# Optimization experiments

Hardware: AMD Instinct MI355X
Metric: run time of the kernel (lower is better)

The kernel has to match this reference:

```python
import jax, jax.numpy as jnp
import numpy as np

BLOCK_SIZE = 1024
OUTLIER_SIGMA = 3.0
OUT_FEATURES = 11008
IN_FEATURES = 4096
TOKENS = 64


def _quantize_mixed_np(W):
    """Faithful numpy port of quantize_mixed (BLOCK_SIZE divides numel exactly here)."""
    flat = W.astype(np.float32).reshape(-1)
    nb = flat.size // BLOCK_SIZE
    blocks = flat.reshape(nb, BLOCK_SIZE)
    mu = blocks.mean(axis=1, keepdims=True)
    sig = np.maximum(blocks.std(axis=1, ddof=1, keepdims=True), 1e-8)  # torch.std is unbiased
    outlier = np.abs(blocks - mu) > OUTLIER_SIGMA * sig
    abs_max = np.maximum(np.abs(np.where(outlier, 0.0, blocks)).max(axis=1), 1e-8)
    scales = (abs_max / 127.0).astype(np.float16)
    q = np.clip(np.round(blocks / abs_max[:, None] * 127.0), -127, 127).astype(np.int8)
    all_pos = np.arange(nb, dtype=np.int64)[:, None] * BLOCK_SIZE + np.arange(BLOCK_SIZE, dtype=np.int64)[None, :]
    int8_data = q[~outlier]                      # row-major == torch order
    fp16_data = blocks[outlier].astype(np.float16)
    int8_pos = all_pos[~outlier].astype(np.int32)
    fp16_pos = all_pos[outlier].astype(np.int32)
    block_idx = np.nonzero(~outlier)[0].astype(np.int32)  # block index per int8 value
    return int8_data, fp16_data, scales, int8_pos, fp16_pos, block_idx


def setup_inputs() -> dict:
    key = jax.random.key(0)
    k_x, k_b = jax.random.split(key)
    rng = np.random.default_rng(0)
    W = (rng.standard_normal((OUT_FEATURES, IN_FEATURES)) * 0.02).astype(np.float32)
    int8_data, fp16_data, scales, int8_pos, fp16_pos, block_idx = _quantize_mixed_np(W)
    x = jax.random.normal(k_x, (TOKENS, IN_FEATURES), dtype=jnp.float16)
    bias = jax.random.normal(k_b, (OUT_FEATURES,), dtype=jnp.float16) * jnp.float16(0.02)
    return {
        "x": x,
        "int8_data": jnp.asarray(int8_data),
        "fp16_data": jnp.asarray(fp16_data),
        "scales": jnp.asarray(scales),
        "bias": bias,
        "int8_pos": jnp.asarray(int8_pos),
        "fp16_pos": jnp.asarray(fp16_pos),
        "block_idx": jnp.asarray(block_idx),
    }


def reference(x, int8_data, fp16_data, scales, bias, int8_pos, fp16_pos, block_idx):
    out_features = bias.shape[0]
    in_features = x.shape[1]
    numel = out_features * in_features  # divisible by BLOCK_SIZE for these dims
    # dequantize_mixed: scatter fp16 outliers and dequantized int8 values into flat fp16 buffer
    flat = jnp.zeros((numel,), dtype=jnp.float16)
    flat = flat.at[fp16_pos].set(fp16_data)
    flat = flat.at[int8_pos].set(int8_data.astype(jnp.float16) * scales[block_idx])
    W = flat.reshape(out_features, in_features)
    # F.linear(x, W, bias) in fp16
    return jnp.dot(x.astype(jnp.float16), W.T) + bias
```

## Files before the change

kernel.cpp:

```cpp
#include <hip/hip_runtime.h>
#include <hip/hip_fp16.h>

#define TOK   64
#define INF   4096
#define OUTF  11008
#define NUMEL (OUTF * INF)
#define NSLC  (NUMEL / 64)
#define NBLK  (OUTF / 16)
#define KSPL  4
#define NCH   4
#define OUTN  (TOK * OUTF)

typedef __attribute__((ext_vector_type(8))) _Float16 half8;
typedef __attribute__((ext_vector_type(4))) _Float16 half4;
typedef __attribute__((ext_vector_type(4))) float floatx4;
typedef __attribute__((ext_vector_type(4), aligned(4))) int int4u;
typedef __attribute__((ext_vector_type(4))) int int4a;

#define BPAD 264

__global__ __launch_bounds__(256) void precompute_kernel(
    const float* __restrict__ x, const int* __restrict__ fppos, int nf,
    _Float16* __restrict__ x16, int* __restrict__ meta) {
  const int t = blockIdx.x * 256 + threadIdx.x;
  if (t < (TOK * INF) / 4) {
    const floatx4 f = *(const floatx4*)&x[t * 4];
    half4 h;
    h[0] = (_Float16)f[0]; h[1] = (_Float16)f[1];
    h[2] = (_Float16)f[2]; h[3] = (_Float16)f[3];
    *(half4*)&x16[t * 4] = h;
  }
  if (t < NSLC) {
    const int target = t << 6;
    int lo = 0, hi = nf;
    while (lo < hi) {
      const int mid = (lo + hi) >> 1;
      if (fppos[mid] < target) lo = mid + 1; else hi = mid;
    }
    unsigned long long mask = 0ull;
    int j = lo;
    while (j < nf) {
      const int d = fppos[j] - target;
      if (d >= 64) break;
      mask |= 1ull << d;
      ++j;
    }
    int4a mv;
    mv[0] = lo;
    mv[1] = (int)(unsigned)(mask & 0xffffffffu);
    mv[2] = (int)(unsigned)(mask >> 32);
    mv[3] = 0;
    *(int4a*)&meta[t * 4] = mv;
  }
}

__device__ __forceinline__ void meta_window(const int p0, const int4a mv,
                                            int& i0, unsigned& m8) {
  const unsigned mlo = (unsigned)mv[1];
  const unsigned mhi = (unsigned)mv[2];
  const int off = p0 & 63;
  m8 = 0xffu & (off < 32 ? (mlo >> off) : (mhi >> (off - 32)));
  const unsigned bl = (off >= 32) ? mlo : (mlo & ((1u << off) - 1u));
  const unsigned bh = (off >= 32) ? (mhi & ((1u << (off - 32)) - 1u)) : 0u;
  i0 = p0 - mv[0] - (__popc(bl) + __popc(bh));
}

__device__ __forceinline__ half8 finish_slot(
    const unsigned m8, const int i0, const int p0, const float s,
    const int (&l)[8], const int* __restrict__ i8,
    const float* __restrict__ fpdat, const int n8) {
  const int f = (int)m8;
  float ov[8];
#pragma unroll
  for (int e = 0; e < 8; ++e) ov[e] = 0.f;
  if (f) {
    int fi = p0 - i0;
#pragma unroll
    for (int e = 0; e < 8; ++e) {
      if ((f >> e) & 1) { ov[e] = fpdat[fi]; ++fi; }
    }
  }

  half8 oh;
  if (i0 + 8 <= n8) {
    if (f == 0) {
#pragma unroll
      for (int e = 0; e < 8; ++e) oh[e] = (_Float16)((float)l[e] * s);
    } else {
      int q = 0;
#pragma unroll
      for (int e = 0; e < 8; ++e) {
        const int flg = (f >> e) & 1;
        int lv = l[0];
#pragma unroll
        for (int qq = 1; qq < 8; ++qq) lv = (q == qq) ? l[qq] : lv;
        oh[e] = flg ? (_Float16)ov[e] : (_Float16)((float)lv * s);
        q += 1 - flg;
      }
    }
  } else {
    int c = 0;
    const int m = n8 - 1;
#pragma unroll
    for (int e = 0; e < 8; ++e) {
      const int flg = (f >> e) & 1;
      int idx = i0 + e - c;
      idx = idx < 0 ? 0 : (idx > m ? m : idx);
      oh[e] = flg ? (_Float16)ov[e] : (_Float16)((float)i8[idx] * s);
      c += flg;
    }
  }
  return oh;
}

__global__ __launch_bounds__(256, 4) void gemm_fused(
    const _Float16* __restrict__ x16, const int* __restrict__ i8,
    const float* __restrict__ fpdat, const float* __restrict__ scales,
    const int* __restrict__ meta, float* __restrict__ part, const int n8) {
  __shared__ __attribute__((aligned(16))) char smem[2 * 16 * BPAD * 2];
  _Float16 (* __restrict__ Bt)[16][BPAD] = (_Float16 (*)[16][BPAD])smem;
  float* red = (float*)smem;

  const int tid  = threadIdx.x;
  const int wave = tid >> 6;
  const int lane = tid & 63;
  const int quad = lane >> 4;
  const int ln   = lane & 15;
  const int nt   = blockIdx.x >> 2;
  const int kq   = blockIdx.x & 3;
  const int n0   = nt << 4;
  const int kbas = kq * 1024;

  int rL[2], k8o[2];
#pragma unroll
  for (int i = 0; i < 2; ++i) {
    const int slot = i * 256 + tid;
    rL[i]  = slot >> 5;
    k8o[i] = (slot & 31) * 8;
  }

  int4a    mreg[2][2];
  float    sreg[2][2];
  int      lreg[2][8];
  int      i0v[2];
  unsigned m8v[2];

#pragma unroll
  for (int i = 0; i < 2; ++i) {
    const int p0 = (n0 + rL[i]) * INF + kbas + k8o[i];
    mreg[0][i] = *(const int4a*)&meta[(p0 >> 6) * 4];
    sreg[0][i] = scales[p0 >> 10];
  }
#pragma unroll
  for (int i = 0; i < 2; ++i) {
    const int p0 = (n0 + rL[i]) * INF + kbas + 256 + k8o[i];
    mreg[1][i] = *(const int4a*)&meta[(p0 >> 6) * 4];
    sreg[1][i] = scales[p0 >> 10];
  }
#pragma unroll
  for (int i = 0; i < 2; ++i) {
    const int p0 = (n0 + rL[i]) * INF + kbas + k8o[i];
    meta_window(p0, mreg[0][i], i0v[i], m8v[i]);
    if (i0v[i] + 8 <= n8) {
      *(int4u*)&lreg[i][0] = *(const int4u*)&i8[i0v[i]];
      *(int4u*)&lreg[i][4] = *(const int4u*)&i8[i0v[i] + 4];
    }
  }
#pragma unroll
  for (int i = 0; i < 2; ++i) {
    const int p0 = (n0 + rL[i]) * INF + kbas + k8o[i];
    const half8 oh = finish_slot(m8v[i], i0v[i], p0, sreg[0][i], lreg[i],
                                 i8, fpdat, n8);
    *(half8*)&Bt[0][rL[i]][k8o[i]] = oh;
  }
  __syncthreads();

  floatx4 acc0 = {0,0,0,0}, acc1 = {0,0,0,0}, acc2 = {0,0,0,0}, acc3 = {0,0,0,0};

#pragma unroll
  for (int c = 0; c < NCH; ++c) {
    const int cur = c & 1;

    if (c + 1 < NCH) {
      const int bk = (c + 1) & 1;
#pragma unroll
      for (int i = 0; i < 2; ++i) {
        const int p0 = (n0 + rL[i]) * INF + kbas + (c + 1) * 256 + k8o[i];
        meta_window(p0, mreg[bk][i], i0v[i], m8v[i]);
        if (i0v[i] + 8 <= n8) {
          *(int4u*)&lreg[i][0] = *(const int4u*)&i8[i0v[i]];
          *(int4u*)&lreg[i][4] = *(const int4u*)&i8[i0v[i] + 4];
        }
      }
      if (c + 2 < NCH) {
        const int bk2 = c & 1;
#pragma unroll
        for (int i = 0; i < 2; ++i) {
          const int p0 = (n0 + rL[i]) * INF + kbas + (c + 2) * 256 + k8o[i];
          mreg[bk2][i] = *(const int4a*)&meta[(p0 >> 6) * 4];
          sreg[bk2][i] = scales[p0 >> 10];
        }
      }
    }

    {
      const _Float16* ap = &x16[ln * INF + kbas + c * 256 + wave * 64 + quad * 8];
      const _Float16* bp = &Bt[cur][ln][wave * 64 + quad * 8];
#pragma unroll
      for (int st = 0; st < 2; ++st) {
        const int ko = st * 32;
        const half8 bh = *(const half8*)&bp[ko];
        const half8 a0 = *(const half8*)&ap[ko];
        const half8 a1 = *(const half8*)&ap[16 * INF + ko];
        const half8 a2 = *(const half8*)&ap[32 * INF + ko];
        const half8 a3 = *(const half8*)&ap[48 * INF + ko];
        acc0 = __builtin_amdgcn_mfma_f32_16x16x32_f16(a0, bh, acc0, 0, 0, 0);
        acc1 = __builtin_amdgcn_mfma_f32_16x16x32_f16(a1, bh, acc1, 0, 0, 0);
        acc2 = __builtin_amdgcn_mfma_f32_16x16x32_f16(a2, bh, acc2, 0, 0, 0);
        acc3 = __builtin_amdgcn_mfma_f32_16x16x32_f16(a3, bh, acc3, 0, 0, 0);
      }
    }

    if (c + 1 < NCH) {
      const int bk = (c + 1) & 1;
      half8 oh[2];
#pragma unroll
      for (int i = 0; i < 2; ++i) {
        const int p0 = (n0 + rL[i]) * INF + kbas + (c + 1) * 256 + k8o[i];
        oh[i] = finish_slot(m8v[i], i0v[i], p0, sreg[bk][i], lreg[i],
                            i8, fpdat, n8);
      }
#pragma unroll
      for (int i = 0; i < 2; ++i)
        *(half8*)&Bt[bk][rL[i]][k8o[i]] = oh[i];
      __syncthreads();
    }
  }
  __syncthreads();

  const int mb = quad * 4;
#pragma unroll
  for (int i = 0; i < 4; ++i) red[wave * 1024 + (mb + i)      * 16 + ln] = acc0[i];
#pragma unroll
  for (int i = 0; i < 4; ++i) red[wave * 1024 + (16 + mb + i) * 16 + ln] = acc1[i];
#pragma unroll
  for (int i = 0; i < 4; ++i) red[wave * 1024 + (32 + mb + i) * 16 + ln] = acc2[i];
#pragma unroll
  for (int i = 0; i < 4; ++i) red[wave * 1024 + (48 + mb + i) * 16 + ln] = acc3[i];
  __syncthreads();

  float* pp = &part[(size_t)kq * OUTN];
#pragma unroll
  for (int c2 = 0; c2 < 4; ++c2) {
    const int cell = tid + c2 * 256;
    const int mm = cell >> 4, nn = cell & 15;
    pp[mm * OUTF + n0 + nn] =
        red[cell] + red[1024 + cell] + red[2048 + cell] + red[3072 + cell];
  }
}

__global__ __launch_bounds__(256) void reduce_kernel(
    const float* __restrict__ part, const float* __restrict__ bias,
    float* __restrict__ out) {
  const int t  = blockIdx.x * 256 + threadIdx.x;
  const int i4 = t * 4;
  floatx4 a = *(const floatx4*)&part[i4];
#pragma unroll
  for (int k = 1; k < KSPL; ++k) {
    const floatx4 b = *(const floatx4*)&part[(size_t)k * OUTN + i4];
    a[0] += b[0]; a[1] += b[1]; a[2] += b[2]; a[3] += b[3];
  }
  const int nn = i4 % OUTF;
  const floatx4 bb = *(const floatx4*)&bias[nn];
  a[0] += bb[0]; a[1] += bb[1]; a[2] += bb[2]; a[3] += bb[3];
  *(floatx4*)&out[i4] = a;
}

extern "C" void kernel_launch(void* const* d_in, const int* in_sizes, int n_in,
                              void* d_out, int out_size, void* d_ws,
                              size_t ws_size, hipStream_t stream) {
  const float* x      = (const float*)d_in[0];
  const int*   i8     = (const int*)d_in[1];
  const float* fpdat  = (const float*)d_in[2];
  const float* scales = (const float*)d_in[3];
  const float* bias   = (const float*)d_in[4];
  const int*   fppos  = (const int*)d_in[6];

  char* wsp = (char*)d_ws;
  _Float16* x16  = (_Float16*)wsp;
  int*      meta = (int*)(wsp + (size_t)TOK * INF * sizeof(_Float16));
  float*    part = (float*)(wsp + (size_t)TOK * INF * sizeof(_Float16)
                                + (size_t)NSLC * 16);
  float*    out  = (float*)d_out;

  const int n8 = in_sizes[1];
  const int nf = in_sizes[2];

  precompute_kernel<<<NSLC / 256, 256, 0, stream>>>(x, fppos, nf, x16, meta);
  gemm_fused<<<NBLK * KSPL, 256, 0, stream>>>(x16, i8, fpdat, scales, meta,
                                              part, n8);
  reduce_kernel<<<OUTN / (4 * 256), 256, 0, stream>>>(part, bias, out);
}
```

Measured before the change: 460.5 us.

## Give each wave a private K-slice tile to drop block-wide barriers

Each wave now owns a contiguous 256-wide K slice and dequantizes its own 16x64 B tile per chunk into a per-wave LDS buffer. This removes the __syncthreads between chunks, since the data is produced and consumed within one wave. Each lane handles 16 consecutive weights through a new window16 helper that computes two 8-wide outlier windows from a single meta word. The per-row scale is loaded once. The cost is more LDS and a dequant step that sits serially before the MFMAs of the same chunk, which reduces overlap.

```diff
diff --git a/kernel.cpp b/kernel.cpp
--- a/kernel.cpp
+++ b/kernel.cpp
@@ -17,7 +17,7 @@
 typedef __attribute__((ext_vector_type(4), aligned(4))) int int4u;
 typedef __attribute__((ext_vector_type(4))) int int4a;
 
-#define BPAD 264
+#define TPAD 72
 
 __global__ __launch_bounds__(256) void precompute_kernel(
     const float* __restrict__ x, const int* __restrict__ fppos, int nf,
@@ -54,15 +54,21 @@
   }
 }
 
-__device__ __forceinline__ void meta_window(const int p0, const int4a mv,
-                                            int& i0, unsigned& m8) {
+__device__ __forceinline__ void window16(const int p0, const int4a mv,
+                                         int& i0a, unsigned& m8a,
+                                         int& i0b, unsigned& m8b) {
   const unsigned mlo = (unsigned)mv[1];
   const unsigned mhi = (unsigned)mv[2];
   const int off = p0 & 63;
-  m8 = 0xffu & (off < 32 ? (mlo >> off) : (mhi >> (off - 32)));
-  const unsigned bl = (off >= 32) ? mlo : (mlo & ((1u << off) - 1u));
-  const unsigned bh = (off >= 32) ? (mhi & ((1u << (off - 32)) - 1u)) : 0u;
-  i0 = p0 - mv[0] - (__popc(bl) + __popc(bh));
+  const unsigned w32 = (off & 32) ? mhi : mlo;
+  const unsigned m16 = (off & 16) ? (w32 >> 16) : (w32 & 0xffffu);
+  int ltb = 0;
+  if (off & 32) ltb += __popc(mlo);
+  if (off & 16) ltb += __popc(w32 & 0xffffu);
+  m8a = m16 & 0xffu;
+  m8b = (m16 >> 8) & 0xffu;
+  i0a = p0 - mv[0] - ltb;
+  i0b = i0a + 8 - __popc(m8a);
 }
 
 __device__ __forceinline__ half8 finish_slot(
@@ -117,95 +123,82 @@
     const _Float16* __restrict__ x16, const int* __restrict__ i8,
     const float* __restrict__ fpdat, const float* __restrict__ scales,
     const int* __restrict__ meta, float* __restrict__ part, const int n8) {
-  __shared__ __attribute__((aligned(16))) char smem[2 * 16 * BPAD * 2];
-  _Float16 (* __restrict__ Bt)[16][BPAD] = (_Float16 (*)[16][BPAD])smem;
+  __shared__ __attribute__((aligned(16))) char smem[4 * 2 * 16 * TPAD * 2];
+  _Float16 (* __restrict__ tiles)[2][16][TPAD] = (_Float16 (*)[2][16][TPAD])smem;
   float* red = (float*)smem;
 
   const int tid  = threadIdx.x;
   const int wave = tid >> 6;
   const int lane = tid & 63;
-  const int quad = lane >> 4;
-  const int ln   = lane & 15;
   const int nt   = blockIdx.x >> 2;
   const int kq   = blockIdx.x & 3;
   const int n0   = nt << 4;
-  const int kbas = kq * 1024;
-
-  int rL[2], k8o[2];
-#pragma unroll
-  for (int i = 0; i < 2; ++i) {
-    const int slot = i * 256 + tid;
-    rL[i]  = slot >> 5;
-    k8o[i] = (slot & 31) * 8;
-  }
-
-  int4a    mreg[2][2];
-  float    sreg[2][2];
-  int      lreg[2][8];
-  int      i0v[2];
-  unsigned m8v[2];
-
-#pragma unroll
-  for (int i = 0; i < 2; ++i) {
-    const int p0 = (n0 + rL[i]) * INF + kbas + k8o[i];
-    mreg[0][i] = *(const int4a*)&meta[(p0 >> 6) * 4];
-    sreg[0][i] = scales[p0 >> 10];
-  }
-#pragma unroll
-  for (int i = 0; i < 2; ++i) {
-    const int p0 = (n0 + rL[i]) * INF + kbas + 256 + k8o[i];
-    mreg[1][i] = *(const int4a*)&meta[(p0 >> 6) * 4];
-    sreg[1][i] = scales[p0 >> 10];
-  }
-#pragma unroll
-  for (int i = 0; i < 2; ++i) {
-    const int p0 = (n0 + rL[i]) * INF + kbas + k8o[i];
-    meta_window(p0, mreg[0][i], i0v[i], m8v[i]);
-    if (i0v[i] + 8 <= n8) {
-      *(int4u*)&lreg[i][0] = *(const int4u*)&i8[i0v[i]];
-      *(int4u*)&lreg[i][4] = *(const int4u*)&i8[i0v[i] + 4];
-    }
-  }
-#pragma unroll
-  for (int i = 0; i < 2; ++i) {
-    const int p0 = (n0 + rL[i]) * INF + kbas + k8o[i];
-    const half8 oh = finish_slot(m8v[i], i0v[i], p0, sreg[0][i], lreg[i],
-                                 i8, fpdat, n8);
-    *(half8*)&Bt[0][rL[i]][k8o[i]] = oh;
-  }
-  __syncthreads();
+  const int kbas = kq * 1024 + wave * 256;
+
+  const int srow  = lane >> 2;
+  const int ssub  = lane & 3;
+  const int prow  = n0 + srow;
+  const int pbase = prow * INF + kbas;
+  const float s   = scales[prow * 4 + kq];
+
+  const int ln   = lane & 15;
+  const int quad = lane >> 4;
+
+  int4a    mreg[2];
+  int      l8[2][16];
+  int      i0a[2], i0b[2];
+  unsigned m8a[2], m8b[2];
+
+  mreg[0] = *(const int4a*)&meta[(pbase >> 6) * 4];
+  mreg[1] = *(const int4a*)&meta[((pbase + 64) >> 6) * 4];
+  {
+    const int p0 = pbase + ssub * 16;
+    window16(p0, mreg[0], i0a[0], m8a[0], i0b[0], m8b[0]);
+    if (i0a[0] + 8 <= n8) {
+      *(int4u*)&l8[0][0] = *(const int4u*)&i8[i0a[0]];
+      *(int4u*)&l8[0][4] = *(const int4u*)&i8[i0a[0] + 4];
+    }
+    if (i0b[0] + 8 <= n8) {
+      *(int4u*)&l8[0][8]  = *(const int4u*)&i8[i0b[0]];
+      *(int4u*)&l8[0][12] = *(const int4u*)&i8[i0b[0] + 4];
+    }
+  }
 
   floatx4 acc0 = {0,0,0,0}, acc1 = {0,0,0,0}, acc2 = {0,0,0,0}, acc3 = {0,0,0,0};
 
 #pragma unroll
   for (int c = 0; c < NCH; ++c) {
-    const int cur = c & 1;
+    const int bk = c & 1;
+    const int nb = bk ^ 1;
 
     if (c + 1 < NCH) {
-      const int bk = (c + 1) & 1;
-#pragma unroll
-      for (int i = 0; i < 2; ++i) {
-        const int p0 = (n0 + rL[i]) * INF + kbas + (c + 1) * 256 + k8o[i];
-        meta_window(p0, mreg[bk][i], i0v[i], m8v[i]);
-        if (i0v[i] + 8 <= n8) {
-          *(int4u*)&lreg[i][0] = *(const int4u*)&i8[i0v[i]];
-          *(int4u*)&lreg[i][4] = *(const int4u*)&i8[i0v[i] + 4];
-        }
-      }
-      if (c + 2 < NCH) {
-        const int bk2 = c & 1;
-#pragma unroll
-        for (int i = 0; i < 2; ++i) {
-          const int p0 = (n0 + rL[i]) * INF + kbas + (c + 2) * 256 + k8o[i];
-          mreg[bk2][i] = *(const int4a*)&meta[(p0 >> 6) * 4];
-          sreg[bk2][i] = scales[p0 >> 10];
-        }
-      }
+      const int p0 = pbase + (c + 1) * 64 + ssub * 16;
+      window16(p0, mreg[nb], i0a[nb], m8a[nb], i0b[nb], m8b[nb]);
+      if (i0a[nb] + 8 <= n8) {
+        *(int4u*)&l8[nb][0] = *(const int4u*)&i8[i0a[nb]];
+        *(int4u*)&l8[nb][4] = *(const int4u*)&i8[i0a[nb] + 4];
+      }
+      if (i0b[nb] + 8 <= n8) {
+        *(int4u*)&l8[nb][8]  = *(const int4u*)&i8[i0b[nb]];
+        *(int4u*)&l8[nb][12] = *(const int4u*)&i8[i0b[nb] + 4];
+      }
+      if (c + 2 < NCH)
+        mreg[bk] = *(const int4a*)&meta[((pbase + (c + 2) * 64) >> 6) * 4];
     }
 
     {
-      const _Float16* ap = &x16[ln * INF + kbas + c * 256 + wave * 64 + quad * 8];
-      const _Float16* bp = &Bt[cur][ln][wave * 64 + quad * 8];
+      const int p0 = pbase + c * 64 + ssub * 16;
+      const half8 ha = finish_slot(m8a[bk], i0a[bk], p0, s,
+                                   *(const int (*)[8])&l8[bk][0], i8, fpdat, n8);
+      const half8 hb = finish_slot(m8b[bk], i0b[bk], p0 + 8, s,
+                                   *(const int (*)[8])&l8[bk][8], i8, fpdat, n8);
+      *(half8*)&tiles[wave][bk][srow][ssub * 16]     = ha;
+      *(half8*)&tiles[wave][bk][srow][ssub * 16 + 8] = hb;
+    }
+
+    {
+      const _Float16* ap = &x16[ln * INF + kbas + c * 64 + quad * 8];
+      const _Float16* bp = &tiles[wave][bk][ln][quad * 8];
 #pragma unroll
       for (int st = 0; st < 2; ++st) {
         const int ko = st * 32;
@@ -220,22 +213,8 @@
         acc3 = __builtin_amdgcn_mfma_f32_16x16x32_f16(a3, bh, acc3, 0, 0, 0);
       }
     }
-
-    if (c + 1 < NCH) {
-      const int bk = (c + 1) & 1;
-      half8 oh[2];
-#pragma unroll
-      for (int i = 0; i < 2; ++i) {
-        const int p0 = (n0 + rL[i]) * INF + kbas + (c + 1) * 256 + k8o[i];
-        oh[i] = finish_slot(m8v[i], i0v[i], p0, sreg[bk][i], lreg[i],
-                            i8, fpdat, n8);
-      }
-#pragma unroll
-      for (int i = 0; i < 2; ++i)
-        *(half8*)&Bt[bk][rL[i]][k8o[i]] = oh[i];
-      __syncthreads();
-    }
-  }
+  }
+
   __syncthreads();
 
   const int mb = quad * 4;
```

New measurement: 1.092 ms. 137% more time.
